# Kernel optimization log

Measured on AMD Instinct MI355X. Metric: run time of the kernel, lower is better.

Reference implementation:

```python
import jax, jax.numpy as jnp
import numpy as np

N = 10000        # nodes
E = 320000       # edges (avg degree 32)
NF_IN = 256
NF_OUT = 512
EPS = 1e-5


def batch_norm(x, gamma, beta):
    # BatchNorm1d training-mode: biased stats over the node (batch) dim
    mu = jnp.mean(x, axis=0)
    var = jnp.var(x, axis=0)
    return (x - mu) * jax.lax.rsqrt(var + EPS) * gamma + beta


def sage_conv(x, src, dst, W_l, W_r, bias):
    # PyG SAGEConv, aggr='mean': out = lin_l(mean_{j->i} x_j) + lin_r(x_i)
    msg = x[src]                                             # [E, F]
    s = jax.ops.segment_sum(msg, dst, num_segments=N)        # [N, F]
    cnt = jax.ops.segment_sum(jnp.ones((msg.shape[0], 1), x.dtype), dst, num_segments=N)
    mean = s / jnp.maximum(cnt, 1.0)
    return mean @ W_l + bias + x @ W_r


def setup_inputs() -> dict:
    key = jax.random.key(0)
    ks = jax.random.split(key, 8)
    x = jax.random.normal(ks[0], (N, NF_IN), jnp.float32)
    edge_index = jax.random.randint(ks[1], (2, E), 0, N, dtype=jnp.int64)
    s_in = 0.02
    return {
        "x": x,
        "edge_index": edge_index,
        "gamma0": jnp.ones((NF_IN,), jnp.float32),
        "beta0": jnp.zeros((NF_IN,), jnp.float32),
        "W0_l": jax.random.normal(ks[2], (NF_IN, NF_OUT), jnp.float32) * s_in,
        "W0_r": jax.random.normal(ks[3], (NF_IN, NF_OUT), jnp.float32) * s_in,
        "bias0": jnp.zeros((NF_OUT,), jnp.float32),
        "gamma1": jnp.ones((NF_OUT,), jnp.float32),
        "beta1": jnp.zeros((NF_OUT,), jnp.float32),
        "W1_l": jax.random.normal(ks[4], (NF_OUT, NF_OUT), jnp.float32) * s_in,
        "W1_r": jax.random.normal(ks[5], (NF_OUT, NF_OUT), jnp.float32) * s_in,
        "bias1": jnp.zeros((NF_OUT,), jnp.float32),
        "W_sc": jax.random.normal(ks[6], (NF_IN, NF_OUT), jnp.float32) * s_in,
        "b_sc": jnp.zeros((NF_OUT,), jnp.float32),
    }


def reference(x, edge_index, gamma0, beta0, W0_l, W0_r, bias0,
              gamma1, beta1, W1_l, W1_r, bias1, W_sc, b_sc):
    src, dst = edge_index[0], edge_index[1]
    h = jax.nn.relu(batch_norm(x, gamma0, beta0))
    h = sage_conv(h, src, dst, W0_l, W0_r, bias0)
    h = jax.nn.relu(batch_norm(h, gamma1, beta1))
    h = sage_conv(h, src, dst, W1_l, W1_r, bias1)
    x_sc = x @ W_sc + b_sc  # nin_shortcut since nf_in != nf_out
    return x_sc + h
```

## Files before the change

### kernel.cpp

```cpp
#include <hip/hip_runtime.h>
#include <hip/hip_bf16.h>
#include <cstdint>
#include <cstddef>

#define N_NODES 10000
#define N_EDGES 320000
#define FIN 256
#define FOUT 512
#define BN_EPS 1e-5f
#define DEG_CAP 96
#define SLICE_CAP 18
#define NRANGES 20
#define NSLICES 16
#define NODES_PER_RANGE (N_NODES / NRANGES)
#define EDGES_PER_SLICE (N_EDGES / NSLICES)
#define SCAN_BLOCKS (NRANGES * NSLICES)

typedef unsigned short ushort_t;
typedef unsigned char uchar_t;
typedef __attribute__((ext_vector_type(8))) short short8;
typedef __attribute__((ext_vector_type(16))) float f32x16;
typedef __attribute__((ext_vector_type(2))) float f32x2;
typedef __attribute__((ext_vector_type(4))) unsigned short ushort4v;
typedef __attribute__((ext_vector_type(8))) unsigned short ushort8v;

__device__ inline ushort_t f2bf(float f) {
  __hip_bfloat16 h = __float2bfloat16(f);
  return *reinterpret_cast<ushort_t*>(&h);
}
__device__ inline float bf2f(ushort_t u) {
  union { unsigned int i; float f; } c;
  c.i = ((unsigned int)u) << 16;
  return c.f;
}
__device__ inline uchar_t f2q(float v) {
  return (uchar_t)(__builtin_amdgcn_cvt_pk_fp8_f32(v, v, 0u, false) & 0xffu);
}
__device__ inline void q4_to_f32(unsigned int w, float* o) {
  f32x2 lo = __builtin_amdgcn_cvt_pk_f32_fp8(w, false);
  f32x2 hi = __builtin_amdgcn_cvt_pk_f32_fp8(w, true);
  o[0] = lo[0]; o[1] = lo[1]; o[2] = hi[0]; o[3] = hi[1];
}
__device__ inline void gload_lds16(const void* g, void* l) {
  __builtin_amdgcn_global_load_lds(
      (const __attribute__((address_space(1))) unsigned int*)g,
      (__attribute__((address_space(3))) unsigned int*)l, 16, 0, 0);
}

__global__ void zero_k(int* __restrict__ p, int n) {
  int i = blockIdx.x * blockDim.x + threadIdx.x;
  if (i < n) p[i] = 0;
}

__global__ __launch_bounds__(256)
void prologue_k(const int* __restrict__ src, const int* __restrict__ dst,
                int* __restrict__ fill, int* __restrict__ csrc,
                const float* __restrict__ W0l, const float* __restrict__ W0r,
                const float* __restrict__ Wsc, const float* __restrict__ W1l,
                const float* __restrict__ W1r, const float* __restrict__ bias1,
                const float* __restrict__ bsc,
                ushort_t* __restrict__ w0lt, ushort_t* __restrict__ w0rt,
                ushort_t* __restrict__ wsct, ushort_t* __restrict__ w1lt,
                ushort_t* __restrict__ w1rt, float* __restrict__ cbias,
                const float* __restrict__ x, float* __restrict__ sums0,
                ushort_t* __restrict__ xb, uchar_t* __restrict__ xq) {
  __shared__ __align__(16) char smem[512 * 4 + NODES_PER_RANGE * SLICE_CAP * 4];
  int b = blockIdx.x;
  int tid = threadIdx.x;

  if (b < SCAN_BLOCKS) {
    int range = b / NSLICES;
    int slice = b % NSLICES;
    int lo = range * NODES_PER_RANGE;
    int* lcnt = (int*)smem;
    int* lbuf = lcnt + 512;
    for (int i = tid; i < NODES_PER_RANGE; i += 256) lcnt[i] = 0;
    __syncthreads();

    int e0 = slice * EDGES_PER_SLICE;
    const int4* dst4 = (const int4*)(dst + e0);
    const int4* src4 = (const int4*)(src + e0);
    const int nvec = EDGES_PER_SLICE / 4;
    for (int v = tid; v < nvec; v += 256) {
      int4 d4 = dst4[v];
      int4 s4 = src4[v];
      int dd[4] = {d4.x, d4.y, d4.z, d4.w};
      int ss[4] = {s4.x, s4.y, s4.z, s4.w};
#pragma unroll
      for (int j = 0; j < 4; ++j) {
        int d = dd[j] - lo;
        if (d >= 0 && d < NODES_PER_RANGE) {
          int pos = atomicAdd(&lcnt[d], 1);
          if (pos < SLICE_CAP) lbuf[d * SLICE_CAP + pos] = ss[j];
        }
      }
    }
    __syncthreads();

    for (int i = tid; i < NODES_PER_RANGE; i += 256) {
      int cnt = min(lcnt[i], SLICE_CAP);
      if (cnt > 0) {
        int off = atomicAdd(&fill[lo + i], cnt);
        int wmax = min(cnt, DEG_CAP - off);
        for (int k = 0; k < wmax; ++k)
          csrc[(size_t)(lo + i) * DEG_CAP + off + k] = lbuf[i * SLICE_CAP + k];
      }
    }
    return;
  }

  if (b < SCAN_BLOCKS + 897) {
    int bb = b - SCAN_BLOCKS;
    if (bb == 896) {
      cbias[tid] = bias1[tid] + bsc[tid];
      cbias[tid + 256] = bias1[tid + 256] + bsc[tid + 256];
      return;
    }
    const float* W;
    ushort_t* Wt;
    int K, t;
    if (bb < 384) {
      K = 256; t = bb & 127;
      if (bb < 128)      { W = W0l; Wt = w0lt; }
      else if (bb < 256) { W = W0r; Wt = w0rt; }
      else               { W = Wsc; Wt = wsct; }
    } else {
      K = 512; t = (bb - 384) & 255;
      if (bb < 640) { W = W1l; Wt = w1lt; }
      else          { W = W1r; Wt = w1rt; }
    }
    ushort_t (*tl)[40] = (ushort_t(*)[40])smem;
    int Kt = K >> 5;
    int bk = (t % Kt) * 32, bn = (t / Kt) * 32;
    int tx = tid & 31, ty = tid >> 5;
#pragma unroll
    for (int i = 0; i < 4; ++i)
      tl[ty + i * 8][tx] = f2bf(W[(size_t)(bk + ty + i * 8) * 512 + bn + tx]);
    __syncthreads();
#pragma unroll
    for (int i = 0; i < 4; ++i)
      Wt[(size_t)(bn + ty + i * 8) * K + bk + tx] = tl[tx][ty + i * 8];
    return;
  }

  int blk = b - (SCAN_BLOCKS + 897);
  int c = tid;
  int r0 = blk * 80, r1 = r0 + 80;
  float s = 0.f, q = 0.f;
  for (int r = r0; r < r1; ++r) {
    float v = x[(size_t)r * FIN + c];
    s += v;
    q = fmaf(v, v, q);
    xb[(size_t)r * FIN + c] = f2bf(v);
    xq[(size_t)r * FIN + c] = f2q(v);
  }
  atomicAdd(&sums0[c], s);
  atomicAdd(&sums0[FIN + c], q);
}

template <int F, bool OWNF32>
__global__ __launch_bounds__(64)
void gather_mean_q8(const uchar_t* __restrict__ H, const int* __restrict__ fill,
                    const int* __restrict__ csrc, const float* __restrict__ sums,
                    const float* __restrict__ gamma, const float* __restrict__ beta,
                    float invN, ushort_t* __restrict__ agg,
                    const void* __restrict__ ownsrc, ushort_t* __restrict__ ownout) {
  constexpr int VEC = F / 64;
  int node = blockIdx.x;
  int c0 = threadIdx.x * VEC;
  float sc[VEC], sh[VEC];
#pragma unroll
  for (int j = 0; j < VEC; ++j) {
    float mu = sums[c0 + j] * invN;
    float var = fmaf(-mu, mu, sums[F + c0 + j] * invN);
    float s = rsqrtf(var + BN_EPS) * gamma[c0 + j];
    sc[j] = s;
    sh[j] = fmaf(-mu, s, beta[c0 + j]);
  }
  if constexpr (OWNF32) {
    const float* xr = (const float*)ownsrc + (size_t)node * F + c0;
    ushort4v o;
#pragma unroll
    for (int j = 0; j < VEC; ++j) o[j] = f2bf(fmaxf(fmaf(xr[j], sc[j], sh[j]), 0.f));
    *(ushort4v*)&ownout[(size_t)node * F + c0] = o;
  } else {
    ushort8v iv = *(const ushort8v*)((const ushort_t*)ownsrc + (size_t)node * F + c0);
    ushort8v o;
#pragma unroll
    for (int j = 0; j < VEC; ++j) o[j] = f2bf(fmaxf(fmaf(bf2f(iv[j]), sc[j], sh[j]), 0.f));
    *(ushort8v*)&ownout[(size_t)node * F + c0] = o;
  }

  int deg = fill[node];
  int lim = min(deg, DEG_CAP);
  const int* cs = csrc + (size_t)node * DEG_CAP;
  float acc[VEC] = {};
  int e = 0;
  for (; e + 2 <= lim; e += 2) {
    int s0 = cs[e], s1 = cs[e + 1];
    float va[VEC], vb[VEC];
    if constexpr (VEC == 8) {
      uint2 ua = *(const uint2*)&H[(size_t)s0 * F + c0];
      uint2 ub = *(const uint2*)&H[(size_t)s1 * F + c0];
      q4_to_f32(ua.x, va); q4_to_f32(ua.y, va + 4);
      q4_to_f32(ub.x, vb); q4_to_f32(ub.y, vb + 4);
    } else {
      unsigned int ua = *(const unsigned int*)&H[(size_t)s0 * F + c0];
      unsigned int ub = *(const unsigned int*)&H[(size_t)s1 * F + c0];
      q4_to_f32(ua, va);
      q4_to_f32(ub, vb);
    }
#pragma unroll
    for (int j = 0; j < VEC; ++j)
      acc[j] += fmaxf(fmaf(va[j], sc[j], sh[j]), 0.f) +
                fmaxf(fmaf(vb[j], sc[j], sh[j]), 0.f);
  }
  if (e < lim) {
    int s0 = cs[e];
    float va[VEC];
    if constexpr (VEC == 8) {
      uint2 ua = *(const uint2*)&H[(size_t)s0 * F + c0];
      q4_to_f32(ua.x, va); q4_to_f32(ua.y, va + 4);
    } else {
      unsigned int ua = *(const unsigned int*)&H[(size_t)s0 * F + c0];
      q4_to_f32(ua, va);
    }
#pragma unroll
    for (int j = 0; j < VEC; ++j) acc[j] += fmaxf(fmaf(va[j], sc[j], sh[j]), 0.f);
  }
  float ic = 1.0f / fmaxf((float)deg, 1.0f);
  if constexpr (VEC == 8) {
    ushort8v o;
#pragma unroll
    for (int j = 0; j < 8; ++j) o[j] = f2bf(acc[j] * ic);
    *(ushort8v*)&agg[(size_t)node * F + c0] = o;
  } else {
    ushort4v o;
#pragma unroll
    for (int j = 0; j < 4; ++j) o[j] = f2bf(acc[j] * ic);
    *(ushort4v*)&agg[(size_t)node * F + c0] = o;
  }
}

template <int EPI, int K0, int K1, int K2, bool STATS, bool WQ>
__global__ __launch_bounds__(256)
void gemm_mfma(const ushort_t* __restrict__ A0p, const ushort_t* __restrict__ B0p,
               const ushort_t* __restrict__ A1p, const ushort_t* __restrict__ B1p,
               const ushort_t* __restrict__ A2p, const ushort_t* __restrict__ B2p,
               const float* __restrict__ bias, void* __restrict__ Cv,
               uchar_t* __restrict__ Cq, int M, float* __restrict__ statsOut) {
  constexpr int ABYTES = 64 * 128;
  constexpr int BBYTES = 128 * 128;
  __shared__ __align__(16) char Asm[2 * ABYTES];
  __shared__ __align__(16) char Bsm[2 * BBYTES];

  int wgid = blockIdx.x;
  int cxcd = wgid & 7;
  int j = wgid >> 3;
  int nt = j & 3;
  int y = cxcd + (j >> 2) * 8;
  int MT = (M + 63) >> 6;
  if (y >= MT) return;
  int m0 = y * 64;
  int n0 = nt * 128;

  int tid = threadIdx.x;
  int lane = tid & 63;
  int w = tid >> 6;
  int wm = w >> 1, wn = w & 1;

  constexpr int NS = (K0 + K1 + K2) / 64;
  f32x16 acc0 = {}, acc1 = {};

  int wbase = (tid & ~63) * 16;

  auto STAGE = [&](int buf, int ks) {
    int k0_ = ks * 64;
    const ushort_t* Ap;
    const ushort_t* Bp;
    int lk, KA;
    if (k0_ < K0) { Ap = A0p; Bp = B0p; lk = k0_; KA = K0; }
    else if (k0_ < K0 + K1) { Ap = A1p; Bp = B1p; lk = k0_ - K0; KA = K1; }
    else { Ap = A2p; Bp = B2p; lk = k0_ - K0 - K1; KA = K2; }
#pragma unroll
    for (int i = 0; i < 2; ++i) {
      int o = i * 4096 + tid * 16;
      int row = o >> 7;
      int chunk = (o >> 4) & 7;
      const ushort_t* g = Ap + (size_t)(m0 + row) * KA + lk + ((chunk ^ (row & 7)) << 3);
      gload_lds16(g, Asm + buf * ABYTES + i * 4096 + wbase);
    }
#pragma unroll
    for (int i = 0; i < 4; ++i) {
      int o = i * 4096 + tid * 16;
      int row = o >> 7;
      int chunk = (o >> 4) & 7;
      const ushort_t* g = Bp + (size_t)(n0 + row) * KA + lk + ((chunk ^ (row & 7)) << 3);
      gload_lds16(g, Bsm + buf * BBYTES + i * 4096 + wbase);
    }
  };

  int arow = wm * 32 + (lane & 31);
  int brow0 = wn * 64 + (lane & 31);
  int brow1 = brow0 + 32;
  int aswzr = (arow & 7) << 4;
  int bswzr = (brow0 & 7) << 4;

  STAGE(0, 0);
  __syncthreads();

  for (int ks = 0; ks < NS; ++ks) {
    if (ks + 1 < NS) STAGE((ks + 1) & 1, ks + 1);
    int abase = (ks & 1) * ABYTES + arow * 128;
    int bbase0 = (ks & 1) * BBYTES + brow0 * 128;
    int bbase1 = (ks & 1) * BBYTES + brow1 * 128;
#pragma unroll
    for (int kc = 0; kc < 4; ++kc) {
      int kb = kc * 32 + (lane >> 5) * 16;
      short8 af = *(const short8*)(Asm + abase + (kb ^ aswzr));
      short8 bf0 = *(const short8*)(Bsm + bbase0 + (kb ^ bswzr));
      short8 bf1 = *(const short8*)(Bsm + bbase1 + (kb ^ bswzr));
      acc0 = __builtin_amdgcn_mfma_f32_32x32x16_bf16(af, bf0, acc0, 0, 0, 0);
      acc1 = __builtin_amdgcn_mfma_f32_32x32x16_bf16(af, bf1, acc1, 0, 0, 0);
    }
    __syncthreads();
  }

  float* st = (float*)Asm;
  if constexpr (STATS) {
    if (tid < 256) st[tid] = 0.f;
    __syncthreads();
  }

  int colb = n0 + wn * 64 + (lane & 31);
  int rquad = (lane >> 5) * 4;
#pragma unroll
  for (int ni = 0; ni < 2; ++ni) {
    int col = colb + ni * 32;
    float bv = bias[col];
    float s_l = 0.f, q_l = 0.f;
#pragma unroll
    for (int reg = 0; reg < 16; ++reg) {
      int row = m0 + wm * 32 + (reg & 3) + 8 * (reg >> 2) + rquad;
      if (row < M) {
        float v = (ni == 0 ? acc0[reg] : acc1[reg]) + bv;
        if constexpr (STATS) {
          s_l += v;
          q_l = fmaf(v, v, q_l);
        }
        if constexpr (EPI == 0) {
          ((ushort_t*)Cv)[(size_t)row * 512 + col] = f2bf(v);
          if constexpr (WQ) Cq[(size_t)row * 512 + col] = f2q(v);
        } else {
          ((float*)Cv)[(size_t)row * 512 + col] = v;
        }
      }
    }
    if constexpr (STATS) {
      int cloc = wn * 64 + ni * 32 + (lane & 31);
      atomicAdd(&st[cloc], s_l);
      atomicAdd(&st[128 + cloc], q_l);
    }
  }
  if constexpr (STATS) {
    __syncthreads();
    if (tid < 256) {
      int c = tid & 127;
      atomicAdd(&statsOut[(tid >> 7) * 512 + n0 + c], st[(tid >> 7) * 128 + c]);
    }
  }
}

extern "C" void kernel_launch(void* const* d_in, const int* in_sizes, int n_in,
                              void* d_out, int out_size, void* d_ws, size_t ws_size,
                              hipStream_t stream) {
  const float* x = (const float*)d_in[0];
  const int* ei = (const int*)d_in[1];
  const int* src = ei;
  const int* dst = ei + N_EDGES;
  const float* gamma0 = (const float*)d_in[2];
  const float* beta0  = (const float*)d_in[3];
  const float* W0l    = (const float*)d_in[4];
  const float* W0r    = (const float*)d_in[5];
  const float* bias0  = (const float*)d_in[6];
  const float* gamma1 = (const float*)d_in[7];
  const float* beta1  = (const float*)d_in[8];
  const float* W1l    = (const float*)d_in[9];
  const float* W1r    = (const float*)d_in[10];
  const float* bias1  = (const float*)d_in[11];
  const float* Wsc    = (const float*)d_in[12];
  const float* bsc    = (const float*)d_in[13];
  float* out = (float*)d_out;

  char* wp = (char*)d_ws;
  ushort_t* agg0b = (ushort_t*)wp; wp += (size_t)N_NODES * FIN * 2;
  ushort_t* h0rb  = (ushort_t*)wp; wp += (size_t)N_NODES * FIN * 2;
  ushort_t* h1b   = (ushort_t*)wp; wp += (size_t)N_NODES * FOUT * 2;
  ushort_t* h1rb  = (ushort_t*)wp; wp += (size_t)N_NODES * FOUT * 2;
  ushort_t* agg1b = (ushort_t*)wp; wp += (size_t)N_NODES * FOUT * 2;
  ushort_t* xb    = (ushort_t*)wp; wp += (size_t)N_NODES * FIN * 2;
  uchar_t*  xq    = (uchar_t*)wp;  wp += (size_t)N_NODES * FIN;
  uchar_t*  h1q   = (uchar_t*)wp;  wp += (size_t)N_NODES * FOUT;
  ushort_t* w0lt  = (ushort_t*)wp; wp += (size_t)FIN * FOUT * 2;
  ushort_t* w0rt  = (ushort_t*)wp; wp += (size_t)FIN * FOUT * 2;
  ushort_t* wsct  = (ushort_t*)wp; wp += (size_t)FIN * FOUT * 2;
  ushort_t* w1lt  = (ushort_t*)wp; wp += (size_t)FOUT * FOUT * 2;
  ushort_t* w1rt  = (ushort_t*)wp; wp += (size_t)FOUT * FOUT * 2;
  float* cbias = (float*)wp; wp += FOUT * 4;
  float* sums0 = (float*)wp; wp += 2 * FIN * 4;
  float* sums1 = (float*)wp; wp += 2 * FOUT * 4;
  int* fill    = (int*)wp; wp += (size_t)N_NODES * 4;
  int* csrc    = (int*)wp; wp += (size_t)N_NODES * DEG_CAP * 4;

  const float invN = 1.0f / N_NODES;

  const int zwords = 2 * FIN + 2 * FOUT + N_NODES;
  zero_k<<<(zwords + 255) / 256, 256, 0, stream>>>((int*)sums0, zwords);

  prologue_k<<<SCAN_BLOCKS + 897 + 125, 256, 0, stream>>>(
      src, dst, fill, csrc, W0l, W0r, Wsc, W1l, W1r, bias1, bsc,
      w0lt, w0rt, wsct, w1lt, w1rt, cbias, x, sums0, xb, xq);

  gather_mean_q8<FIN, true><<<N_NODES, 64, 0, stream>>>(
      xq, fill, csrc, sums0, gamma0, beta0, invN, agg0b, x, h0rb);

  const int GEMM_GRID = 8 * 4 * ((((N_NODES + 63) / 64) + 7) / 8);

  gemm_mfma<0, FIN, FIN, 0, true, true>
      <<<GEMM_GRID, 256, 0, stream>>>(
      agg0b, w0lt, h0rb, w0rt, nullptr, nullptr, bias0, h1b, h1q, N_NODES, sums1);

  gather_mean_q8<FOUT, false><<<N_NODES, 64, 0, stream>>>(
      h1q, fill, csrc, sums1, gamma1, beta1, invN, agg1b, h1b, h1rb);

  gemm_mfma<1, FOUT, FOUT, FIN, false, false>
      <<<GEMM_GRID, 256, 0, stream>>>(
      agg1b, w1lt, h1rb, w1rt, xb, wsct, cbias, out, nullptr, N_NODES, nullptr);
}
```

Baseline: 115.4 us.

## Use per-slice adjacency buckets and split GEMM K across 8 waves

The adjacency build now writes each slice's neighbor list into a fixed per-(node,slice) bucket with a byte count, instead of appending into a shared per-node list through global atomics. This removes the atomics and the fill-array zeroing, but the gather loop now walks 16 small slices per node. The GEMM kernel moves to 512 threads, with two wave groups each handling half of every K step, followed by a reduction of partial accumulators through LDS. The split K is meant to raise per-block parallelism and latency hiding, at the cost of an extra LDS reduction and barrier.

```diff
diff --git a/kernel.cpp b/kernel.cpp
--- a/kernel.cpp
+++ b/kernel.cpp
@@ -8,7 +8,6 @@
 #define FIN 256
 #define FOUT 512
 #define BN_EPS 1e-5f
-#define DEG_CAP 96
 #define SLICE_CAP 18
 #define NRANGES 20
 #define NSLICES 16
@@ -54,7 +53,7 @@
 
 __global__ __launch_bounds__(256)
 void prologue_k(const int* __restrict__ src, const int* __restrict__ dst,
-                int* __restrict__ fill, int* __restrict__ csrc,
+                uchar_t* __restrict__ scnt, int* __restrict__ csrc,
                 const float* __restrict__ W0l, const float* __restrict__ W0r,
                 const float* __restrict__ Wsc, const float* __restrict__ W1l,
                 const float* __restrict__ W1r, const float* __restrict__ bias1,
@@ -99,12 +98,9 @@
 
     for (int i = tid; i < NODES_PER_RANGE; i += 256) {
       int cnt = min(lcnt[i], SLICE_CAP);
-      if (cnt > 0) {
-        int off = atomicAdd(&fill[lo + i], cnt);
-        int wmax = min(cnt, DEG_CAP - off);
-        for (int k = 0; k < wmax; ++k)
-          csrc[(size_t)(lo + i) * DEG_CAP + off + k] = lbuf[i * SLICE_CAP + k];
-      }
+      scnt[(size_t)(lo + i) * NSLICES + slice] = (uchar_t)cnt;
+      int* dp = csrc + ((size_t)(lo + i) * NSLICES + slice) * SLICE_CAP;
+      for (int k = 0; k < cnt; ++k) dp[k] = lbuf[i * SLICE_CAP + k];
     }
     return;
   }
@@ -160,7 +156,7 @@
 
 template <int F, bool OWNF32>
 __global__ __launch_bounds__(64)
-void gather_mean_q8(const uchar_t* __restrict__ H, const int* __restrict__ fill,
+void gather_mean_q8(const uchar_t* __restrict__ H, const uchar_t* __restrict__ scnt,
                     const int* __restrict__ csrc, const float* __restrict__ sums,
                     const float* __restrict__ gamma, const float* __restrict__ beta,
                     float invN, ushort_t* __restrict__ agg,
@@ -191,42 +187,54 @@
     *(ushort8v*)&ownout[(size_t)node * F + c0] = o;
   }
 
-  int deg = fill[node];
-  int lim = min(deg, DEG_CAP);
-  const int* cs = csrc + (size_t)node * DEG_CAP;
+  const uchar_t* sp = scnt + (size_t)node * NSLICES;
+  uint4 sw = *(const uint4*)sp;
+  int deg = 0;
+  {
+    unsigned wds[4] = {sw.x, sw.y, sw.z, sw.w};
+#pragma unroll
+    for (int qd = 0; qd < 4; ++qd)
+      deg += (int)((wds[qd] & 0xff) + ((wds[qd] >> 8) & 0xff) +
+                   ((wds[qd] >> 16) & 0xff) + ((wds[qd] >> 24) & 0xff));
+  }
+
   float acc[VEC] = {};
-  int e = 0;
-  for (; e + 2 <= lim; e += 2) {
-    int s0 = cs[e], s1 = cs[e + 1];
-    float va[VEC], vb[VEC];
-    if constexpr (VEC == 8) {
-      uint2 ua = *(const uint2*)&H[(size_t)s0 * F + c0];
-      uint2 ub = *(const uint2*)&H[(size_t)s1 * F + c0];
-      q4_to_f32(ua.x, va); q4_to_f32(ua.y, va + 4);
-      q4_to_f32(ub.x, vb); q4_to_f32(ub.y, vb + 4);
-    } else {
-      unsigned int ua = *(const unsigned int*)&H[(size_t)s0 * F + c0];
-      unsigned int ub = *(const unsigned int*)&H[(size_t)s1 * F + c0];
-      q4_to_f32(ua, va);
-      q4_to_f32(ub, vb);
-    }
-#pragma unroll
-    for (int j = 0; j < VEC; ++j)
-      acc[j] += fmaxf(fmaf(va[j], sc[j], sh[j]), 0.f) +
-                fmaxf(fmaf(vb[j], sc[j], sh[j]), 0.f);
-  }
-  if (e < lim) {
-    int s0 = cs[e];
-    float va[VEC];
-    if constexpr (VEC == 8) {
-      uint2 ua = *(const uint2*)&H[(size_t)s0 * F + c0];
-      q4_to_f32(ua.x, va); q4_to_f32(ua.y, va + 4);
-    } else {
-      unsigned int ua = *(const unsigned int*)&H[(size_t)s0 * F + c0];
-      q4_to_f32(ua, va);
-    }
-#pragma unroll
-    for (int j = 0; j < VEC; ++j) acc[j] += fmaxf(fmaf(va[j], sc[j], sh[j]), 0.f);
+  for (int s = 0; s < NSLICES; ++s) {
+    int cnt = sp[s];
+    const int* cs = csrc + ((size_t)node * NSLICES + s) * SLICE_CAP;
+    int e = 0;
+    for (; e + 2 <= cnt; e += 2) {
+      int s0 = cs[e], s1 = cs[e + 1];
+      float va[VEC], vb[VEC];
+      if constexpr (VEC == 8) {
+        uint2 ua = *(const uint2*)&H[(size_t)s0 * F + c0];
+        uint2 ub = *(const uint2*)&H[(size_t)s1 * F + c0];
+        q4_to_f32(ua.x, va); q4_to_f32(ua.y, va + 4);
+        q4_to_f32(ub.x, vb); q4_to_f32(ub.y, vb + 4);
+      } else {
+        unsigned int ua = *(const unsigned int*)&H[(size_t)s0 * F + c0];
+        unsigned int ub = *(const unsigned int*)&H[(size_t)s1 * F + c0];
+        q4_to_f32(ua, va);
+        q4_to_f32(ub, vb);
+      }
+#pragma unroll
+      for (int j = 0; j < VEC; ++j)
+        acc[j] += fmaxf(fmaf(va[j], sc[j], sh[j]), 0.f) +
+                  fmaxf(fmaf(vb[j], sc[j], sh[j]), 0.f);
+    }
+    if (e < cnt) {
+      int s0 = cs[e];
+      float va[VEC];
+      if constexpr (VEC == 8) {
+        uint2 ua = *(const uint2*)&H[(size_t)s0 * F + c0];
+        q4_to_f32(ua.x, va); q4_to_f32(ua.y, va + 4);
+      } else {
+        unsigned int ua = *(const unsigned int*)&H[(size_t)s0 * F + c0];
+        q4_to_f32(ua, va);
+      }
+#pragma unroll
+      for (int j = 0; j < VEC; ++j) acc[j] += fmaxf(fmaf(va[j], sc[j], sh[j]), 0.f);
+    }
   }
   float ic = 1.0f / fmaxf((float)deg, 1.0f);
   if constexpr (VEC == 8) {
@@ -243,7 +251,7 @@
 }
 
 template <int EPI, int K0, int K1, int K2, bool STATS, bool WQ>
-__global__ __launch_bounds__(256)
+__global__ __launch_bounds__(512)
 void gemm_mfma(const ushort_t* __restrict__ A0p, const ushort_t* __restrict__ B0p,
                const ushort_t* __restrict__ A1p, const ushort_t* __restrict__ B1p,
                const ushort_t* __restrict__ A2p, const ushort_t* __restrict__ B2p,
@@ -267,7 +275,8 @@
   int tid = threadIdx.x;
   int lane = tid & 63;
   int w = tid >> 6;
-  int wm = w >> 1, wn = w & 1;
+  int wk = w >> 2;
+  int wm = (w >> 1) & 1, wn = w & 1;
 
   constexpr int NS = (K0 + K1 + K2) / 64;
   f32x16 acc0 = {}, acc1 = {};
@@ -282,21 +291,20 @@
     if (k0_ < K0) { Ap = A0p; Bp = B0p; lk = k0_; KA = K0; }
     else if (k0_ < K0 + K1) { Ap = A1p; Bp = B1p; lk = k0_ - K0; KA = K1; }
     else { Ap = A2p; Bp = B2p; lk = k0_ - K0 - K1; KA = K2; }
-#pragma unroll
-    for (int i = 0; i < 2; ++i) {
-      int o = i * 4096 + tid * 16;
+    {
+      int o = tid * 16;
       int row = o >> 7;
       int chunk = (o >> 4) & 7;
       const ushort_t* g = Ap + (size_t)(m0 + row) * KA + lk + ((chunk ^ (row & 7)) << 3);
-      gload_lds16(g, Asm + buf * ABYTES + i * 4096 + wbase);
-    }
-#pragma unroll
-    for (int i = 0; i < 4; ++i) {
-      int o = i * 4096 + tid * 16;
+      gload_lds16(g, Asm + buf * ABYTES + wbase);
+    }
+#pragma unroll
+    for (int i = 0; i < 2; ++i) {
+      int o = i * 8192 + tid * 16;
       int row = o >> 7;
       int chunk = (o >> 4) & 7;
       const ushort_t* g = Bp + (size_t)(n0 + row) * KA + lk + ((chunk ^ (row & 7)) << 3);
-      gload_lds16(g, Bsm + buf * BBYTES + i * 4096 + wbase);
+      gload_lds16(g, Bsm + buf * BBYTES + i * 8192 + wbase);
     }
   };
 
@@ -315,7 +323,8 @@
     int bbase0 = (ks & 1) * BBYTES + brow0 * 128;
     int bbase1 = (ks & 1) * BBYTES + brow1 * 128;
 #pragma unroll
-    for (int kc = 0; kc < 4; ++kc) {
+    for (int kc2 = 0; kc2 < 2; ++kc2) {
+      int kc = wk * 2 + kc2;
       int kb = kc * 32 + (lane >> 5) * 16;
       short8 af = *(const short8*)(Asm + abase + (kb ^ aswzr));
       short8 bf0 = *(const short8*)(Bsm + bbase0 + (kb ^ bswzr));
@@ -326,40 +335,62 @@
     __syncthreads();
   }
 
+  float* red = (float*)Bsm;
+  if (w >= 4) {
+    float* r = red + (w - 4) * 2048;
+#pragma unroll
+    for (int t = 0; t < 16; ++t) {
+      r[t * 64 + lane] = acc0[t];
+      r[1024 + t * 64 + lane] = acc1[t];
+    }
+  }
+  __syncthreads();
+  if (w < 4) {
+    const float* r = red + w * 2048;
+#pragma unroll
+    for (int t = 0; t < 16; ++t) {
+      acc0[t] += r[t * 64 + lane];
+      acc1[t] += r[1024 + t * 64 + lane];
+    }
+  }
+
   float* st = (float*)Asm;
   if constexpr (STATS) {
+    __syncthreads();
     if (tid < 256) st[tid] = 0.f;
     __syncthreads();
   }
 
-  int colb = n0 + wn * 64 + (lane & 31);
-  int rquad = (lane >> 5) * 4;
-#pragma unroll
-  for (int ni = 0; ni < 2; ++ni) {
-    int col = colb + ni * 32;
-    float bv = bias[col];
-    float s_l = 0.f, q_l = 0.f;
-#pragma unroll
-    for (int reg = 0; reg < 16; ++reg) {
-      int row = m0 + wm * 32 + (reg & 3) + 8 * (reg >> 2) + rquad;
-      if (row < M) {
-        float v = (ni == 0 ? acc0[reg] : acc1[reg]) + bv;
-        if constexpr (STATS) {
-          s_l += v;
-          q_l = fmaf(v, v, q_l);
-        }
-        if constexpr (EPI == 0) {
-          ((ushort_t*)Cv)[(size_t)row * 512 + col] = f2bf(v);
-          if constexpr (WQ) Cq[(size_t)row * 512 + col] = f2q(v);
-        } else {
-          ((float*)Cv)[(size_t)row * 512 + col] = v;
+  if (w < 4) {
+    int colb = n0 + wn * 64 + (lane & 31);
+    int rquad = (lane >> 5) * 4;
+#pragma unroll
+    for (int ni = 0; ni < 2; ++ni) {
+      int col = colb + ni * 32;
+      float bv = bias[col];
+      float s_l = 0.f, q_l = 0.f;
+#pragma unroll
+      for (int reg = 0; reg < 16; ++reg) {
+        int row = m0 + wm * 32 + (reg & 3) + 8 * (reg >> 2) + rquad;
+        if (row < M) {
+          float v = (ni == 0 ? acc0[reg] : acc1[reg]) + bv;
+          if constexpr (STATS) {
+            s_l += v;
+            q_l = fmaf(v, v, q_l);
+          }
+          if constexpr (EPI == 0) {
+            ((ushort_t*)Cv)[(size_t)row * 512 + col] = f2bf(v);
+            if constexpr (WQ) Cq[(size_t)row * 512 + col] = f2q(v);
+          } else {
+            ((float*)Cv)[(size_t)row * 512 + col] = v;
+          }
         }
       }
-    }
-    if constexpr (STATS) {
-      int cloc = wn * 64 + ni * 32 + (lane & 31);
-      atomicAdd(&st[cloc], s_l);
-      atomicAdd(&st[128 + cloc], q_l);
+      if constexpr (STATS) {
+        int cloc = wn * 64 + ni * 32 + (lane & 31);
+        atomicAdd(&st[cloc], s_l);
+        atomicAdd(&st[128 + cloc], q_l);
+      }
     }
   }
   if constexpr (STATS) {
@@ -409,31 +440,32 @@
   float* cbias = (float*)wp; wp += FOUT * 4;
   float* sums0 = (float*)wp; wp += 2 * FIN * 4;
   float* sums1 = (float*)wp; wp += 2 * FOUT * 4;
-  int* fill    = (int*)wp; wp += (size_t)N_NODES * 4;
-  int* csrc    = (int*)wp; wp += (size_t)N_NODES * DEG_CAP * 4;
+  uchar_t* scnt = (uchar_t*)wp; wp += (size_t)N_NODES * NSLICES;
+  wp = (char*)(((uintptr_t)wp + 15) & ~(uintptr_t)15);
+  int* csrc    = (int*)wp; wp += (size_t)N_NODES * NSLICES * SLICE_CAP * 4;
 
   const float invN = 1.0f / N_NODES;
 
-  const int zwords = 2 * FIN + 2 * FOUT + N_NODES;
-  zero_k<<<(zwords + 255) / 256, 256, 0, stream>>>((int*)sums0, zwords);
+  const int zwords = 2 * FIN + 2 * FOUT;
+  zero_k<<<6, 256, 0, stream>>>((int*)sums0, zwords);
 
   prologue_k<<<SCAN_BLOCKS + 897 + 125, 256, 0, stream>>>(
-      src, dst, fill, csrc, W0l, W0r, Wsc, W1l, W1r, bias1, bsc,
+      src, dst, scnt, csrc, W0l, W0r, Wsc, W1l, W1r, bias1, bsc,
       w0lt, w0rt, wsct, w1lt, w1rt, cbias, x, sums0, xb, xq);
 
   gather_mean_q8<FIN, true><<<N_NODES, 64, 0, stream>>>(
-      xq, fill, csrc, sums0, gamma0, beta0, invN, agg0b, x, h0rb);
+      xq, scnt, csrc, sums0, gamma0, beta0, invN, agg0b, x, h0rb);
 
   const int GEMM_GRID = 8 * 4 * ((((N_NODES + 63) / 64) + 7) / 8);
 
   gemm_mfma<0, FIN, FIN, 0, true, true>
-      <<<GEMM_GRID, 256, 0, stream>>>(
+      <<<GEMM_GRID, 512, 0, stream>>>(
       agg0b, w0lt, h0rb, w0rt, nullptr, nullptr, bias0, h1b, h1q, N_NODES, sums1);
 
   gather_mean_q8<FOUT, false><<<N_NODES, 64, 0, stream>>>(
-      h1q, fill, csrc, sums1, gamma1, beta1, invN, agg1b, h1b, h1rb);
+      h1q, scnt, csrc, sums1, gamma1, beta1, invN, agg1b, h1b, h1rb);
 
   gemm_mfma<1, FOUT, FOUT, FIN, false, false>
-      <<<GEMM_GRID, 256, 0, stream>>>(
+      <<<GEMM_GRID, 512, 0, stream>>>(
       agg1b, w1lt, h1rb, w1rt, xb, wsct, cbias, out, nullptr, N_NODES, nullptr);
 }
```

After: 141.6 us. 22.8% more time.
